# Kernel tuning notes

Hardware: AMD Instinct MI355X
Metric: run time of the kernel (lower is better)

Reference implementation:

```python
import jax, jax.numpy as jnp
import numpy as np

B, S, D = 2, 2048, 1024
H, DH = 16, 64  # num_heads, hidden_dimension (per-head)


def setup_inputs() -> dict:
    key = jax.random.key(0)
    ks = jax.random.split(key, 9)
    s = 1.0 / np.sqrt(D)
    so = 1.0 / np.sqrt(H * DH)
    return {
        "x": jax.random.normal(ks[0], (B, S, D), dtype=jnp.float32),
        "Wq": jax.random.uniform(ks[1], (D, H * DH), jnp.float32, -s, s),
        "bq": jax.random.uniform(ks[2], (H * DH,), jnp.float32, -s, s),
        "Wk": jax.random.uniform(ks[3], (D, H * DH), jnp.float32, -s, s),
        "bk": jax.random.uniform(ks[4], (H * DH,), jnp.float32, -s, s),
        "Wv": jax.random.uniform(ks[5], (D, H * DH), jnp.float32, -s, s),
        "bv": jax.random.uniform(ks[6], (H * DH,), jnp.float32, -s, s),
        "Wo": jax.random.uniform(ks[7], (H * DH, D), jnp.float32, -so, so),
        "bo": jax.random.uniform(ks[8], (D,), jnp.float32, -so, so),
    }


def reference(x, Wq, bq, Wk, bk, Wv, bv, Wo, bo):
    b, s, _ = x.shape
    # project and split heads: [b, h, s, dh]
    q = (x @ Wq + bq).reshape(b, s, H, DH).transpose(0, 2, 1, 3)
    k = (x @ Wk + bk).reshape(b, s, H, DH).transpose(0, 2, 1, 3)
    v = (x @ Wv + bv).reshape(b, s, H, DH).transpose(0, 2, 1, 3)
    scores = jnp.einsum('bhqd,bhkd->bhqk', q, k) / jnp.sqrt(jnp.float32(DH))
    causal = jnp.triu(jnp.ones((s, s), dtype=bool), k=1)
    scores = jnp.where(causal, -jnp.inf, scores)
    weights = jax.nn.softmax(scores, axis=-1)
    out = jnp.einsum('bhqk,bhkd->bhqd', weights, v)
    out = out.transpose(0, 2, 1, 3).reshape(b, s, H * DH)
    return out @ Wo + bo
```

## Files before the change

### kernel.cpp

```cpp
#include <hip/hip_runtime.h>

#define B_  2
#define S_  2048
#define D_  1024
#define H_  16
#define DH_ 64
#define NDH (H_*DH_)
#define BS_ (B_*S_)
#define PER ((size_t)B_*H_*S_*DH_)

typedef __bf16 bf16;
typedef bf16 bf16x8 __attribute__((ext_vector_type(8)));
typedef bf16 bf16x4 __attribute__((ext_vector_type(4)));
typedef float f32x4 __attribute__((ext_vector_type(4)));

#define QSCALE 0.18033688011112042f

#define AS1 __attribute__((address_space(1)))
#define AS3 __attribute__((address_space(3)))
__device__ inline void gld16(const bf16* g, bf16* l) {
    __builtin_amdgcn_global_load_lds((const AS1 void*)g, (AS3 void*)l, 16, 0, 0);
}

__global__ __launch_bounds__(256) void prep(
        const float* __restrict__ x,
        const float* __restrict__ W0, const float* __restrict__ W1,
        const float* __restrict__ W2, const float* __restrict__ W3,
        bf16* __restrict__ xb, bf16* __restrict__ T0, bf16* __restrict__ T1,
        bf16* __restrict__ T2, bf16* __restrict__ T3) {
    __shared__ float T[32][33];
    int bid = blockIdx.x, t = threadIdx.x;
    if (bid < 4096) {
        int i = (bid * 256 + t) * 4;
        float4 v = *(const float4*)(x + i);
        bf16x4 o = { (bf16)v.x, (bf16)v.y, (bf16)v.z, (bf16)v.w };
        *(bf16x4*)(xb + i) = o;
        return;
    }
    int r2 = bid - 4096;
    int z = r2 >> 10, w = r2 & 1023;
    const float* W = (z == 0) ? W0 : (z == 1) ? W1 : (z == 2) ? W2 : W3;
    bf16* Wt = (z == 0) ? T0 : (z == 1) ? T1 : (z == 2) ? T2 : T3;
    int k0 = (w >> 5) * 32, n0 = (w & 31) * 32;
    int r = t >> 3, c = (t & 7) * 4;
    float4 v = *(const float4*)(W + (size_t)(k0 + r) * 1024 + n0 + c);
    T[c + 0][r] = v.x; T[c + 1][r] = v.y; T[c + 2][r] = v.z; T[c + 3][r] = v.w;
    __syncthreads();
    bf16x4 o = { (bf16)T[r][c], (bf16)T[r][c + 1], (bf16)T[r][c + 2], (bf16)T[r][c + 3] };
    *(bf16x4*)(Wt + (size_t)(n0 + r) * 1024 + k0 + c) = o;
}

__global__ __launch_bounds__(256) void qkv_gemm(
        const bf16* __restrict__ A, const bf16* __restrict__ Bt,
        const float* __restrict__ bq, const float* __restrict__ bk,
        const float* __restrict__ bv, bf16* __restrict__ Qout, bf16* __restrict__ Vt) {
    __shared__ __align__(16) bf16 As[2][128 * 32];
    __shared__ __align__(16) bf16 Bs[2][128 * 32];
    int tid = threadIdx.x, wave = tid >> 6, lane = tid & 63;
    int quad = lane >> 4, l16 = lane & 15;

    int flat = blockIdx.y * 24 + blockIdx.x;
    int swz  = (flat & 7) * 96 + (flat >> 3);
    int bm = (swz / 24) * 128, bn = (swz % 24) * 128;
    int wm = (wave >> 1) * 64, wn = (wave & 1) * 64;

    int sr = lane >> 2, sc = (lane & 3) * 8;
    const bf16* Ag0 = A + (size_t)(bm + (wave * 2 + 0) * 16 + sr) * 1024 + sc;
    const bf16* Ag1 = A + (size_t)(bm + (wave * 2 + 1) * 16 + sr) * 1024 + sc;
    const bf16* Bg0 = Bt + (size_t)(bn + (wave * 2 + 0) * 16 + sr) * 1024 + sc;
    const bf16* Bg1 = Bt + (size_t)(bn + (wave * 2 + 1) * 16 + sr) * 1024 + sc;
    int la0 = (wave * 2 + 0) * 512;
    int la1 = (wave * 2 + 1) * 512;

    f32x4 acc[4][4] = {};

    gld16(Ag0, &As[0][la0]);
    gld16(Ag1, &As[0][la1]);
    gld16(Bg0, &Bs[0][la0]);
    gld16(Bg1, &Bs[0][la1]);
    asm volatile("s_waitcnt vmcnt(0)" ::: "memory");
    __builtin_amdgcn_s_barrier();

    for (int t = 0; t < 32; ++t) {
        int cur = t & 1, nxt = cur ^ 1;
        if (t < 31) {
            int k0 = (t + 1) * 32;
            gld16(Ag0 + k0, &As[nxt][la0]);
            gld16(Ag1 + k0, &As[nxt][la1]);
            gld16(Bg0 + k0, &Bs[nxt][la0]);
            gld16(Bg1 + k0, &Bs[nxt][la1]);
        }
        bf16x8 af[4], bfr[4];
        #pragma unroll
        for (int i = 0; i < 4; ++i)
            af[i] = *(const bf16x8*)&As[cur][(wm + i * 16 + l16) * 32 + quad * 8];
        #pragma unroll
        for (int j = 0; j < 4; ++j)
            bfr[j] = *(const bf16x8*)&Bs[cur][(wn + j * 16 + l16) * 32 + quad * 8];
        #pragma unroll
        for (int i = 0; i < 4; ++i)
          #pragma unroll
          for (int j = 0; j < 4; ++j)
            acc[i][j] = __builtin_amdgcn_mfma_f32_16x16x32_bf16(af[i], bfr[j], acc[i][j], 0, 0, 0);
        asm volatile("s_waitcnt vmcnt(0)" ::: "memory");
        __builtin_amdgcn_s_barrier();
    }

    #pragma unroll
    for (int i = 0; i < 4; ++i)
      #pragma unroll
      for (int j = 0; j < 4; ++j) {
        int col = bn + wn + j * 16 + l16;
        float bias = (col < 1024) ? bq[col] : (col < 2048) ? bk[col - 1024] : bv[col - 2048];
        int qkv = col >> 10, cw = col & 1023;
        int hh = cw >> 6, d = cw & 63;
        int row0 = bm + wm + i * 16 + quad * 4;
        int bb = row0 >> 11, s0 = row0 & 2047;
        if (qkv < 2) {
            float scl = (qkv == 0) ? QSCALE : 1.0f;
            #pragma unroll
            for (int r = 0; r < 4; ++r)
                Qout[(size_t)qkv * PER + (((size_t)bb * H_ + hh) * S_ + s0 + r) * DH_ + d] =
                    (bf16)((acc[i][j][r] + bias) * scl);
        } else {
            bf16x4 pack;
            #pragma unroll
            for (int r = 0; r < 4; ++r) pack[r] = (bf16)(acc[i][j][r] + bias);
            *(bf16x4*)&Vt[(((size_t)bb * H_ + hh) * DH_ + d) * S_ + s0] = pack;
        }
      }
}

__global__ __launch_bounds__(256) void gemm_proj(
        const bf16* __restrict__ A, const bf16* __restrict__ Bt,
        const float* __restrict__ bias, float* __restrict__ out) {
    __shared__ __align__(16) bf16 As[2][128 * 32];
    __shared__ __align__(16) bf16 Bs[2][64 * 32];
    int tid = threadIdx.x, wave = tid >> 6, lane = tid & 63;
    int quad = lane >> 4, l16 = lane & 15;

    int flat = blockIdx.y * 16 + blockIdx.x;
    int swz  = (flat & 7) * 64 + (flat >> 3);
    int bm = (swz / 16) * 128, bn = (swz % 16) * 64;
    int wm = (wave >> 1) * 64, wn = (wave & 1) * 32;

    int sr = lane >> 2, sc = (lane & 3) * 8;
    const bf16* Ag0 = A + (size_t)(bm + (wave * 2 + 0) * 16 + sr) * 1024 + sc;
    const bf16* Ag1 = A + (size_t)(bm + (wave * 2 + 1) * 16 + sr) * 1024 + sc;
    const bf16* Bg0 = Bt + (size_t)(bn + wave * 16 + sr) * 1024 + sc;
    int la0 = (wave * 2 + 0) * 512;
    int la1 = (wave * 2 + 1) * 512;
    int lb0 = wave * 512;

    f32x4 acc[4][2] = {};

    gld16(Ag0, &As[0][la0]);
    gld16(Ag1, &As[0][la1]);
    gld16(Bg0, &Bs[0][lb0]);
    asm volatile("s_waitcnt vmcnt(0)" ::: "memory");
    __builtin_amdgcn_s_barrier();

    for (int t = 0; t < 32; ++t) {
        int cur = t & 1, nxt = cur ^ 1;
        if (t < 31) {
            int k0 = (t + 1) * 32;
            gld16(Ag0 + k0, &As[nxt][la0]);
            gld16(Ag1 + k0, &As[nxt][la1]);
            gld16(Bg0 + k0, &Bs[nxt][lb0]);
        }
        bf16x8 af[4], bfr[2];
        #pragma unroll
        for (int i = 0; i < 4; ++i)
            af[i] = *(const bf16x8*)&As[cur][(wm + i * 16 + l16) * 32 + quad * 8];
        #pragma unroll
        for (int j = 0; j < 2; ++j)
            bfr[j] = *(const bf16x8*)&Bs[cur][(wn + j * 16 + l16) * 32 + quad * 8];
        #pragma unroll
        for (int i = 0; i < 4; ++i)
          #pragma unroll
          for (int j = 0; j < 2; ++j)
            acc[i][j] = __builtin_amdgcn_mfma_f32_16x16x32_bf16(af[i], bfr[j], acc[i][j], 0, 0, 0);
        asm volatile("s_waitcnt vmcnt(0)" ::: "memory");
        __builtin_amdgcn_s_barrier();
    }

    #pragma unroll
    for (int i = 0; i < 4; ++i)
      #pragma unroll
      for (int j = 0; j < 2; ++j) {
        int col = bn + wn + j * 16 + l16;
        float b = bias[col];
        #pragma unroll
        for (int r = 0; r < 4; ++r) {
            int row = bm + wm + i * 16 + quad * 4 + r;
            out[(size_t)row * 1024 + col] = acc[i][j][r] + b;
        }
      }
}

__global__ __launch_bounds__(256) void flash4(
        const bf16* __restrict__ Q, const bf16* __restrict__ K,
        const bf16* __restrict__ Vt, bf16* __restrict__ O) {
    int bh = blockIdx.x;
    int b = bh >> 4, h = bh & 15;
    int pr = blockIdx.y;
    int tid = threadIdx.x;
    int wave = tid >> 6, lane = tid & 63;
    int quad = lane >> 4, l16 = lane & 15;

    __shared__ __align__(16) char smem[4 * 2 * 16 * 72 * 2];
    bf16 (*P)[2][16][72] = reinterpret_cast<bf16 (*)[2][16][72]>(smem);
    float (*redO)[4][64][4] = reinterpret_cast<float (*)[4][64][4]>(smem);
    __shared__ float redL[4][2][4][4];

    const bf16* Qb = Q + (size_t)bh * S_ * DH_;
    const bf16* Kb = K + (size_t)bh * S_ * DH_;
    const bf16* Vb = Vt + (size_t)bh * DH_ * S_;

    bf16x8 ones;
    #pragma unroll
    for (int j = 0; j < 8; ++j) ones[j] = (l16 == 0) ? (bf16)1.0f : (bf16)0.0f;

    for (int half = 0; half < 2; ++half) {
        int tile = half ? (63 - pr) : pr;
        int q0 = tile * 32;

        bf16x8 qf[2][2];
        #pragma unroll
        for (int s = 0; s < 2; ++s) {
            const bf16* qp = Qb + (size_t)(q0 + s * 16 + l16) * DH_ + quad * 8;
            qf[s][0] = *(const bf16x8*)(qp);
            qf[s][1] = *(const bf16x8*)(qp + 32);
        }

        f32x4 oacc[2][4] = {};
        f32x4 lacc[2] = {};

        int nkt = tile / 2 + 1;
        for (int kt = wave; kt < nkt; kt += 4) {
            int kv0 = kt * 64;
            bf16x8 kf[4][2];
            #pragma unroll
            for (int ns = 0; ns < 4; ++ns) {
                const bf16* kp = Kb + (size_t)(kv0 + ns * 16 + l16) * DH_ + quad * 8;
                kf[ns][0] = *(const bf16x8*)(kp);
                kf[ns][1] = *(const bf16x8*)(kp + 32);
            }
            f32x4 sacc[2][4] = {};
            #pragma unroll
            for (int s = 0; s < 2; ++s)
              #pragma unroll
              for (int ns = 0; ns < 4; ++ns) {
                sacc[s][ns] = __builtin_amdgcn_mfma_f32_16x16x32_bf16(qf[s][0], kf[ns][0], sacc[s][ns], 0, 0, 0);
                sacc[s][ns] = __builtin_amdgcn_mfma_f32_16x16x32_bf16(qf[s][1], kf[ns][1], sacc[s][ns], 0, 0, 0);
              }
            bool diag = (kt == nkt - 1);
            #pragma unroll
            for (int s = 0; s < 2; ++s)
              #pragma unroll
              for (int ns = 0; ns < 4; ++ns)
                #pragma unroll
                for (int r = 0; r < 4; ++r) {
                    float p = __builtin_amdgcn_exp2f(sacc[s][ns][r]);
                    if (diag) {
                        int kv = kv0 + ns * 16 + l16;
                        int qq = q0 + s * 16 + quad * 4 + r;
                        if (kv > qq) p = 0.f;
                    }
                    P[wave][s][quad * 4 + r][ns * 16 + l16] = (bf16)p;
                }
            #pragma unroll
            for (int ks = 0; ks < 2; ++ks) {
                bf16x8 pf0 = *(const bf16x8*)&P[wave][0][l16][ks * 32 + quad * 8];
                bf16x8 pf1 = *(const bf16x8*)&P[wave][1][l16][ks * 32 + quad * 8];
                lacc[0] = __builtin_amdgcn_mfma_f32_16x16x32_bf16(pf0, ones, lacc[0], 0, 0, 0);
                lacc[1] = __builtin_amdgcn_mfma_f32_16x16x32_bf16(pf1, ones, lacc[1], 0, 0, 0);
                #pragma unroll
                for (int ds = 0; ds < 4; ++ds) {
                    bf16x8 vf = *(const bf16x8*)(Vb + (size_t)(ds * 16 + l16) * S_ + kv0 + ks * 32 + quad * 8);
                    oacc[0][ds] = __builtin_amdgcn_mfma_f32_16x16x32_bf16(pf0, vf, oacc[0][ds], 0, 0, 0);
                    oacc[1][ds] = __builtin_amdgcn_mfma_f32_16x16x32_bf16(pf1, vf, oacc[1][ds], 0, 0, 0);
                }
            }
        }

        if (l16 == 0) {
            #pragma unroll
            for (int s = 0; s < 2; ++s)
              #pragma unroll
              for (int r = 0; r < 4; ++r)
                redL[wave][s][quad][r] = lacc[s][r];
        }
        #pragma unroll
        for (int s = 0; s < 2; ++s) {
            __syncthreads();
            #pragma unroll
            for (int ds = 0; ds < 4; ++ds)
                *(f32x4*)&redO[wave][ds][lane][0] = oacc[s][ds];
            __syncthreads();
            f32x4 osum = {};
            #pragma unroll
            for (int w = 0; w < 4; ++w)
                osum += *(const f32x4*)&redO[w][wave][lane][0];
            #pragma unroll
            for (int r = 0; r < 4; ++r) {
                float lsum = redL[0][s][quad][r] + redL[1][s][quad][r]
                           + redL[2][s][quad][r] + redL[3][s][quad][r];
                int qq = q0 + s * 16 + quad * 4 + r;
                O[((size_t)b * S_ + qq) * NDH + h * DH_ + wave * 16 + l16] = (bf16)(osum[r] / lsum);
            }
        }
        __syncthreads();
    }
}

extern "C" void kernel_launch(void* const* d_in, const int* in_sizes, int n_in,
                              void* d_out, int out_size, void* d_ws, size_t ws_size,
                              hipStream_t stream) {
    const float* x  = (const float*)d_in[0];
    const float* Wq = (const float*)d_in[1];
    const float* bq = (const float*)d_in[2];
    const float* Wk = (const float*)d_in[3];
    const float* bk = (const float*)d_in[4];
    const float* Wv = (const float*)d_in[5];
    const float* bv = (const float*)d_in[6];
    const float* Wo = (const float*)d_in[7];
    const float* bo = (const float*)d_in[8];
    float* out = (float*)d_out;

    bf16* ws = (bf16*)d_ws;
    const size_t M1 = (size_t)1024 * 1024;
    bf16* xb    = ws;
    bf16* WqkvT = ws + 4 * M1;
    bf16* WoT   = ws + 7 * M1;
    bf16* Qw    = ws + 8 * M1;
    bf16* Vtw   = ws + 16 * M1;
    bf16* Ow    = ws + 20 * M1;

    prep<<<8192, 256, 0, stream>>>(x, Wq, Wk, Wv, Wo,
                                   xb, WqkvT, WqkvT + M1, WqkvT + 2 * M1, WoT);

    qkv_gemm<<<dim3(3072 / 128, BS_ / 128), 256, 0, stream>>>(xb, WqkvT, bq, bk, bv, Qw, Vtw);

    flash4<<<dim3(B_ * H_, 32), 256, 0, stream>>>(Qw, Qw + PER, Vtw, Ow);

    gemm_proj<<<dim3(1024 / 64, BS_ / 128), 256, 0, stream>>>(Ow, WoT, bo, out);
}
```

Measured before the change: 220.0 us.

## Split flash attention waves across query subtiles and KV halves

Each wave now owns one 16-row query subtile and strides over half of the KV tiles, instead of every wave processing both subtiles over a quarter of the KV tiles. This halves per-wave accumulator registers and P scratch, and the cross-wave reduction becomes a two-way sum done in a single round with fewer barriers. In exchange each wave loads K and V fragments for only one subtile, so K/V global traffic per block roughly doubles.

```diff
diff --git a/kernel.cpp b/kernel.cpp
--- a/kernel.cpp
+++ b/kernel.cpp
@@ -198,7 +198,7 @@
       }
 }
 
-__global__ __launch_bounds__(256) void flash4(
+__global__ __launch_bounds__(256) void flash9(
         const bf16* __restrict__ Q, const bf16* __restrict__ K,
         const bf16* __restrict__ Vt, bf16* __restrict__ O) {
     int bh = blockIdx.x;
@@ -207,11 +207,12 @@
     int tid = threadIdx.x;
     int wave = tid >> 6, lane = tid & 63;
     int quad = lane >> 4, l16 = lane & 15;
-
-    __shared__ __align__(16) char smem[4 * 2 * 16 * 72 * 2];
-    bf16 (*P)[2][16][72] = reinterpret_cast<bf16 (*)[2][16][72]>(smem);
+    int s = wave & 1, hhalf = wave >> 1;
+
+    __shared__ __align__(16) char smem[16384];
+    bf16 (*P)[16][72] = reinterpret_cast<bf16 (*)[16][72]>(smem);
     float (*redO)[4][64][4] = reinterpret_cast<float (*)[4][64][4]>(smem);
-    __shared__ float redL[4][2][4][4];
+    __shared__ float redL[4][4][4];
 
     const bf16* Qb = Q + (size_t)bh * S_ * DH_;
     const bf16* Kb = K + (size_t)bh * S_ * DH_;
@@ -225,19 +226,18 @@
         int tile = half ? (63 - pr) : pr;
         int q0 = tile * 32;
 
-        bf16x8 qf[2][2];
-        #pragma unroll
-        for (int s = 0; s < 2; ++s) {
+        bf16x8 qf[2];
+        {
             const bf16* qp = Qb + (size_t)(q0 + s * 16 + l16) * DH_ + quad * 8;
-            qf[s][0] = *(const bf16x8*)(qp);
-            qf[s][1] = *(const bf16x8*)(qp + 32);
-        }
-
-        f32x4 oacc[2][4] = {};
-        f32x4 lacc[2] = {};
+            qf[0] = *(const bf16x8*)(qp);
+            qf[1] = *(const bf16x8*)(qp + 32);
+        }
+
+        f32x4 oacc[4] = {};
+        f32x4 lacc = {};
 
         int nkt = tile / 2 + 1;
-        for (int kt = wave; kt < nkt; kt += 4) {
+        for (int kt = hhalf; kt < nkt; kt += 2) {
             int kv0 = kt * 64;
             bf16x8 kf[4][2];
             #pragma unroll
@@ -246,68 +246,57 @@
                 kf[ns][0] = *(const bf16x8*)(kp);
                 kf[ns][1] = *(const bf16x8*)(kp + 32);
             }
-            f32x4 sacc[2][4] = {};
-            #pragma unroll
-            for (int s = 0; s < 2; ++s)
+            f32x4 sacc[4] = {};
+            #pragma unroll
+            for (int ns = 0; ns < 4; ++ns) {
+                sacc[ns] = __builtin_amdgcn_mfma_f32_16x16x32_bf16(qf[0], kf[ns][0], sacc[ns], 0, 0, 0);
+                sacc[ns] = __builtin_amdgcn_mfma_f32_16x16x32_bf16(qf[1], kf[ns][1], sacc[ns], 0, 0, 0);
+            }
+            bool diag = (kt == nkt - 1);
+            #pragma unroll
+            for (int ns = 0; ns < 4; ++ns)
               #pragma unroll
-              for (int ns = 0; ns < 4; ++ns) {
-                sacc[s][ns] = __builtin_amdgcn_mfma_f32_16x16x32_bf16(qf[s][0], kf[ns][0], sacc[s][ns], 0, 0, 0);
-                sacc[s][ns] = __builtin_amdgcn_mfma_f32_16x16x32_bf16(qf[s][1], kf[ns][1], sacc[s][ns], 0, 0, 0);
+              for (int r = 0; r < 4; ++r) {
+                  float p = __builtin_amdgcn_exp2f(sacc[ns][r]);
+                  if (diag) {
+                      int kv = kv0 + ns * 16 + l16;
+                      int qq = q0 + s * 16 + quad * 4 + r;
+                      if (kv > qq) p = 0.f;
+                  }
+                  P[wave][quad * 4 + r][ns * 16 + l16] = (bf16)p;
               }
-            bool diag = (kt == nkt - 1);
-            #pragma unroll
-            for (int s = 0; s < 2; ++s)
-              #pragma unroll
-              for (int ns = 0; ns < 4; ++ns)
-                #pragma unroll
-                for (int r = 0; r < 4; ++r) {
-                    float p = __builtin_amdgcn_exp2f(sacc[s][ns][r]);
-                    if (diag) {
-                        int kv = kv0 + ns * 16 + l16;
-                        int qq = q0 + s * 16 + quad * 4 + r;
-                        if (kv > qq) p = 0.f;
-                    }
-                    P[wave][s][quad * 4 + r][ns * 16 + l16] = (bf16)p;
-                }
             #pragma unroll
             for (int ks = 0; ks < 2; ++ks) {
-                bf16x8 pf0 = *(const bf16x8*)&P[wave][0][l16][ks * 32 + quad * 8];
-                bf16x8 pf1 = *(const bf16x8*)&P[wave][1][l16][ks * 32 + quad * 8];
-                lacc[0] = __builtin_amdgcn_mfma_f32_16x16x32_bf16(pf0, ones, lacc[0], 0, 0, 0);
-                lacc[1] = __builtin_amdgcn_mfma_f32_16x16x32_bf16(pf1, ones, lacc[1], 0, 0, 0);
+                bf16x8 pf = *(const bf16x8*)&P[wave][l16][ks * 32 + quad * 8];
+                lacc = __builtin_amdgcn_mfma_f32_16x16x32_bf16(pf, ones, lacc, 0, 0, 0);
                 #pragma unroll
                 for (int ds = 0; ds < 4; ++ds) {
                     bf16x8 vf = *(const bf16x8*)(Vb + (size_t)(ds * 16 + l16) * S_ + kv0 + ks * 32 + quad * 8);
-                    oacc[0][ds] = __builtin_amdgcn_mfma_f32_16x16x32_bf16(pf0, vf, oacc[0][ds], 0, 0, 0);
-                    oacc[1][ds] = __builtin_amdgcn_mfma_f32_16x16x32_bf16(pf1, vf, oacc[1][ds], 0, 0, 0);
+                    oacc[ds] = __builtin_amdgcn_mfma_f32_16x16x32_bf16(pf, vf, oacc[ds], 0, 0, 0);
                 }
             }
         }
 
+        __syncthreads();
+        #pragma unroll
+        for (int ds = 0; ds < 4; ++ds)
+            *(f32x4*)&redO[wave][ds][lane][0] = oacc[ds];
         if (l16 == 0) {
             #pragma unroll
-            for (int s = 0; s < 2; ++s)
-              #pragma unroll
-              for (int r = 0; r < 4; ++r)
-                redL[wave][s][quad][r] = lacc[s][r];
-        }
-        #pragma unroll
-        for (int s = 0; s < 2; ++s) {
-            __syncthreads();
-            #pragma unroll
-            for (int ds = 0; ds < 4; ++ds)
-                *(f32x4*)&redO[wave][ds][lane][0] = oacc[s][ds];
-            __syncthreads();
-            f32x4 osum = {};
-            #pragma unroll
-            for (int w = 0; w < 4; ++w)
-                osum += *(const f32x4*)&redO[w][wave][lane][0];
+            for (int r = 0; r < 4; ++r)
+                redL[wave][quad][r] = lacc[r];
+        }
+        __syncthreads();
+        #pragma unroll
+        for (int i = 0; i < 2; ++i) {
+            int dsp = hhalf * 2 + i;
+            f32x4 osum = *(const f32x4*)&redO[s][dsp][lane][0];
+            osum += *(const f32x4*)&redO[s + 2][dsp][lane][0];
             #pragma unroll
             for (int r = 0; r < 4; ++r) {
-                float lsum = redL[0][s][quad][r] + redL[1][s][quad][r]
-                           + redL[2][s][quad][r] + redL[3][s][quad][r];
+                float lsum = redL[s][quad][r] + redL[s + 2][quad][r];
                 int qq = q0 + s * 16 + quad * 4 + r;
-                O[((size_t)b * S_ + qq) * NDH + h * DH_ + wave * 16 + l16] = (bf16)(osum[r] / lsum);
+                O[((size_t)b * S_ + qq) * NDH + h * DH_ + dsp * 16 + l16] = (bf16)(osum[r] / lsum);
             }
         }
         __syncthreads();
@@ -342,7 +331,7 @@
 
     qkv_gemm<<<dim3(3072 / 128, BS_ / 128), 256, 0, stream>>>(xb, WqkvT, bq, bk, bv, Qw, Vtw);
 
-    flash4<<<dim3(B_ * H_, 32), 256, 0, stream>>>(Qw, Qw + PER, Vtw, Ow);
+    flash9<<<dim3(B_ * H_, 32), 256, 0, stream>>>(Qw, Qw + PER, Vtw, Ow);
 
     gemm_proj<<<dim3(1024 / 64, BS_ / 128), 256, 0, stream>>>(Ow, WoT, bo, out);
 }
```

Result: slower. 272.6 us (+23.9%).
